# Performance work log

Hardware: AMD Instinct MI355X
Metric: run time of the kernel (lower is better)

Reference implementation:

```python
import jax, jax.numpy as jnp
import numpy as np

D_MODEL = 128
D_STATE = 256
D_CONV = 4
EXPAND = 2
D_INNER = EXPAND * D_MODEL  # 256 == D_STATE (required by the module's einsum/add)
B = 4
L = 100  # fixed: self.C has first dim 100


def silu(x):
    return x * jax.nn.sigmoid(x)


def setup_inputs() -> dict:
    key = jax.random.key(0)
    ks = jax.random.split(key, 10)
    s = 0.02
    dt_std = D_INNER ** (-0.5)
    inp = {
        "hidden_states": jax.random.normal(ks[0], (B, L, D_MODEL), jnp.float32),
        "state": jax.random.normal(ks[1], (B, L, D_INNER, D_STATE), jnp.float32),
        # torch nn.Linear layout: (out_features, in_features)
        "in_proj_w": jax.random.normal(ks[2], (2 * D_INNER, D_MODEL), jnp.float32) * s,
        "in_proj_b": jnp.zeros((2 * D_INNER,), jnp.float32),
        # depthwise conv1d weight: (d_inner, 1, d_conv)
        "conv_w": jax.random.normal(ks[3], (D_INNER, 1, D_CONV), jnp.float32) * s,
        "conv_b": jnp.zeros((D_INNER,), jnp.float32),
        "x_proj_w": jax.random.normal(ks[4], (2 * D_STATE, D_INNER), jnp.float32) * s,
        "dt_proj_w": jax.random.uniform(ks[5], (D_INNER, D_INNER), jnp.float32, -dt_std, dt_std),
        "dt_proj_b": jnp.zeros((D_INNER,), jnp.float32),
        # A_log = log(arange(1, d_state+1)) broadcast to (d_inner, d_state)
        "A_log": jnp.log(jnp.broadcast_to(jnp.arange(1, D_STATE + 1, dtype=jnp.float32), (D_INNER, D_STATE))),
        "D1": jnp.ones((D_INNER,), jnp.float32),
        # torch inits self.C to ones; add tiny noise to avoid degenerate baseline
        "C_param": jnp.ones((L, D_STATE, D_STATE), jnp.float32) + jax.random.normal(ks[6], (L, D_STATE, D_STATE), jnp.float32) * 0.01,
        "out_proj_w": jax.random.normal(ks[7], (D_MODEL, D_INNER), jnp.float32) * s,
        "out_proj_b": jnp.zeros((D_MODEL,), jnp.float32),
    }
    return inp


def reference(hidden_states, state, in_proj_w, in_proj_b, conv_w, conv_b,
              x_proj_w, dt_proj_w, dt_proj_b, A_log, D1, C_param,
              out_proj_w, out_proj_b):
    b, l, _ = hidden_states.shape
    xz = hidden_states @ in_proj_w.T + in_proj_b          # (b, l, 2*d_inner)
    x, z = jnp.split(xz, 2, axis=-1)                      # each (b, l, d_inner)

    # causal depthwise conv: pad (d_conv-1) left == conv with pad both sides then [:, :, :l]
    xc = jnp.transpose(x, (0, 2, 1))                      # (b, d_inner, l)
    xc = jax.lax.conv_general_dilated(
        xc, conv_w, window_strides=(1,), padding=[(conv_w.shape[-1] - 1, 0)],
        dimension_numbers=("NCH", "OIH", "NCH"), feature_group_count=xc.shape[1])
    xc = xc + conv_b[None, :, None]
    x = silu(jnp.transpose(xc, (0, 2, 1)))                # (b, l, d_inner)

    bc = x @ x_proj_w.T                                   # (b, l, 2*d_state)
    Bm, _Cm_unused = jnp.split(bc, 2, axis=-1)            # torch shadows chunked C with self.C

    dt = jax.nn.softplus(x @ dt_proj_w.T + dt_proj_b)     # (b, l, d_inner)
    A = -jnp.exp(A_log)                                   # (d_inner, d_state)
    dA = jnp.exp(dt[..., None] * A)                       # (b, l, d_inner, d_state)
    dB = dt[..., None] * Bm[..., None, :]                 # (b, l, d_inner, d_state)
    actual_state = state * dA + dB                        # elementwise 'blnd,blnd->blnd'

    y = jnp.einsum("bldn,ldn->bln", actual_state, C_param) + D1 * x  # (b, l, d_inner)
    y = y * silu(z)
    out = y @ out_proj_w.T + out_proj_b                   # (b, l, d_model)
    return out, actual_state
```

## Files before the change

### kernel.cpp

```cpp
#include <hip/hip_runtime.h>

#define LEN 100
#define NR 400

__device__ __forceinline__ float siluf_(float x) { return x / (1.0f + __expf(-x)); }
__device__ __forceinline__ float softplusf_(float x) {
    return (x > 20.f) ? x : log1pf(expf(x));
}

typedef float f4v __attribute__((ext_vector_type(4)));
__device__ __forceinline__ float4 nt_load4(const float* p) {
    f4v t = __builtin_nontemporal_load((const f4v*)p);
    return make_float4(t.x, t.y, t.z, t.w);
}
__device__ __forceinline__ void nt_store4(float* p, float4 v) {
    f4v t; t.x = v.x; t.y = v.y; t.z = v.z; t.w = v.w;
    __builtin_nontemporal_store(t, (f4v*)p);
}

__global__ void k_nega(const float* __restrict__ alog, float* __restrict__ negA) {
    int i = blockIdx.x * 256 + threadIdx.x;
    negA[i] = -expf(alog[i]);
}

__global__ void __launch_bounds__(256) k_front(
    const float* __restrict__ hidden, const float* __restrict__ ipw, const float* __restrict__ ipb,
    const float* __restrict__ cw, const float* __restrict__ cb,
    const float* __restrict__ xpw, const float* __restrict__ dtw, const float* __restrict__ dtb,
    float* __restrict__ xact, float* __restrict__ Bm, float* __restrict__ dt,
    float* __restrict__ zs)
{
    int r = blockIdx.x;
    int l = r % LEN;
    int j = threadIdx.x;
    int lb = l < 3 ? l : 3;
    __shared__ float hid[4][128];
    __shared__ __align__(16) float xs[256];

    for (int e = j; e < 512; e += 256) {
        int k = e >> 7;
        int c = e & 127;
        hid[k][c] = (k <= lb) ? hidden[(size_t)(r - k) * 128 + c] : 0.f;
    }
    __syncthreads();

    float b0 = ipb[j];
    float xp0 = b0, xp1 = b0, xp2 = b0, xp3 = b0;
    float z = ipb[256 + j];
    const float* wx = ipw + (size_t)j * 128;
    const float* wz = ipw + (size_t)(256 + j) * 128;
#pragma unroll 8
    for (int c = 0; c < 128; c += 4) {
        float4 w = *(const float4*)(wx + c);
        xp0 += w.x * hid[0][c] + w.y * hid[0][c+1] + w.z * hid[0][c+2] + w.w * hid[0][c+3];
        xp1 += w.x * hid[1][c] + w.y * hid[1][c+1] + w.z * hid[1][c+2] + w.w * hid[1][c+3];
        xp2 += w.x * hid[2][c] + w.y * hid[2][c+1] + w.z * hid[2][c+2] + w.w * hid[2][c+3];
        xp3 += w.x * hid[3][c] + w.y * hid[3][c+1] + w.z * hid[3][c+2] + w.w * hid[3][c+3];
        float4 v = *(const float4*)(wz + c);
        z += v.x * hid[0][c] + v.y * hid[0][c+1] + v.z * hid[0][c+2] + v.w * hid[0][c+3];
    }
    float4 w4 = *(const float4*)(cw + j * 4);
    float conv = cb[j] + w4.w * xp0;
    if (lb >= 1) conv += w4.z * xp1;
    if (lb >= 2) conv += w4.y * xp2;
    if (lb >= 3) conv += w4.x * xp3;
    float xa = siluf_(conv);
    xs[j] = xa;
    xact[r * 256 + j] = xa;
    zs[r * 256 + j] = siluf_(z);
    __syncthreads();

    float accB = 0.f, accD = dtb[j];
    const float* bw = xpw + (size_t)j * 256;
    const float* dw = dtw + (size_t)j * 256;
#pragma unroll 8
    for (int c = 0; c < 256; c += 4) {
        float4 bwv = *(const float4*)(bw + c);
        float4 dwv = *(const float4*)(dw + c);
        float4 xv  = *(const float4*)(xs + c);
        accB += bwv.x * xv.x + bwv.y * xv.y + bwv.z * xv.z + bwv.w * xv.w;
        accD += dwv.x * xv.x + dwv.y * xv.y + dwv.z * xv.z + dwv.w * xv.w;
    }
    Bm[r * 256 + j] = accB;
    dt[r * 256 + j] = softplusf_(accD);
}

__global__ void __launch_bounds__(256, 8) k_scan(
    const float* __restrict__ state, const float* __restrict__ negA,
    const float* __restrict__ Cp, const float* __restrict__ dt,
    const float* __restrict__ Bm, float* __restrict__ ostate, float* __restrict__ ypart)
{
    int bid = blockIdx.x;
    int r = bid >> 3, sl = bid & 7;
    int l = r % LEN;
    int tid = threadIdx.x;
    int wid = tid >> 6, lane = tid & 63, n0 = lane * 4;
    int d0 = sl * 32 + wid * 8;
    const float* dtp = dt + r * 256 + d0;
    float4 Bv = *(const float4*)(Bm + r * 256 + n0);
    const float* sp = state + ((size_t)(r * 256 + d0)) * 256 + n0;
    const float* cp = Cp + ((size_t)(l * 256 + d0)) * 256 + n0;
    const float* ap = negA + (size_t)d0 * 256 + n0;
    float* op = ostate + ((size_t)(r * 256 + d0)) * 256 + n0;

    __shared__ __align__(16) float accs[4][256];

    float4 acc = make_float4(0.f, 0.f, 0.f, 0.f);
    float4 s = nt_load4(sp);
    float4 c = *(const float4*)(cp);
    float4 a = *(const float4*)(ap);
#pragma unroll
    for (int i = 0; i < 8; ++i) {
        float4 s1, c1, a1;
        if (i < 7) {
            s1 = nt_load4(sp + (size_t)(i + 1) * 256);
            c1 = *(const float4*)(cp + (size_t)(i + 1) * 256);
            a1 = *(const float4*)(ap + (size_t)(i + 1) * 256);
        }
        float dtv = dtp[i];
        float4 as;
        as.x = s.x * __expf(dtv * a.x) + dtv * Bv.x;
        as.y = s.y * __expf(dtv * a.y) + dtv * Bv.y;
        as.z = s.z * __expf(dtv * a.z) + dtv * Bv.z;
        as.w = s.w * __expf(dtv * a.w) + dtv * Bv.w;
        nt_store4(op + (size_t)i * 256, as);
        acc.x += as.x * c.x;
        acc.y += as.y * c.y;
        acc.z += as.z * c.z;
        acc.w += as.w * c.w;
        if (i < 7) { s = s1; c = c1; a = a1; }
    }
    *(float4*)(&accs[wid][n0]) = acc;
    __syncthreads();
    if (wid == 0) {
        float4 t0 = *(const float4*)(&accs[0][n0]);
        float4 t1 = *(const float4*)(&accs[1][n0]);
        float4 t2 = *(const float4*)(&accs[2][n0]);
        float4 t3 = *(const float4*)(&accs[3][n0]);
        float4 o;
        o.x = t0.x + t1.x + t2.x + t3.x;
        o.y = t0.y + t1.y + t2.y + t3.y;
        o.z = t0.z + t1.z + t2.z + t3.z;
        o.w = t0.w + t1.w + t2.w + t3.w;
        *(float4*)(ypart + ((size_t)(sl * NR + r)) * 256 + n0) = o;
    }
}

__global__ void __launch_bounds__(256) k_back(
    const float* __restrict__ ypart, const float* __restrict__ xact,
    const float* __restrict__ zs, const float* __restrict__ D1,
    const float* __restrict__ ow, const float* __restrict__ ob,
    float* __restrict__ out)
{
    int r = blockIdx.x;
    int t = threadIdx.x;
    __shared__ __align__(16) float ys[256];
    const int S = NR * 256;
    int idx = r * 256 + t;
    float v = 0.f;
#pragma unroll
    for (int q = 0; q < 8; q++) v += ypart[q * S + idx];
    v += D1[t] * xact[idx];
    v *= zs[idx];
    ys[t] = v;
    __syncthreads();
    if (t < 128) {
        const float* wp = ow + (size_t)t * 256;
        float acc = ob[t];
#pragma unroll 8
        for (int c = 0; c < 256; c += 4) {
            float4 w = *(const float4*)(wp + c);
            float4 x = *(const float4*)(ys + c);
            acc += w.x * x.x + w.y * x.y + w.z * x.z + w.w * x.w;
        }
        out[r * 128 + t] = acc;
    }
}

extern "C" void kernel_launch(void* const* d_in, const int* in_sizes, int n_in,
                              void* d_out, int out_size, void* d_ws, size_t ws_size,
                              hipStream_t stream) {
    const float* hidden = (const float*)d_in[0];
    const float* state  = (const float*)d_in[1];
    const float* ipw    = (const float*)d_in[2];
    const float* ipb    = (const float*)d_in[3];
    const float* cw     = (const float*)d_in[4];
    const float* cb     = (const float*)d_in[5];
    const float* xpw    = (const float*)d_in[6];
    const float* dtw    = (const float*)d_in[7];
    const float* dtb    = (const float*)d_in[8];
    const float* alog   = (const float*)d_in[9];
    const float* D1     = (const float*)d_in[10];
    const float* Cp     = (const float*)d_in[11];
    const float* opw    = (const float*)d_in[12];
    const float* opb    = (const float*)d_in[13];

    float* out    = (float*)d_out;
    float* ostate = out + 51200;

    float* ws    = (float*)d_ws;
    float* negA  = ws;
    float* xact  = ws + 65536;
    float* Bm    = ws + 167936;
    float* dt    = ws + 270336;
    float* zs    = ws + 372736;
    float* ypart = ws + 475136;

    k_nega <<<256,  256, 0, stream>>>(alog, negA);
    k_front<<<400,  256, 0, stream>>>(hidden, ipw, ipb, cw, cb, xpw, dtw, dtb,
                                      xact, Bm, dt, zs);
    k_scan <<<3200, 256, 0, stream>>>(state, negA, Cp, dt, Bm, ostate, ypart);
    k_back <<<400,  256, 0, stream>>>(ypart, xact, zs, D1, opw, opb, out);
}
```

Baseline: 288.9 us.

## Share C_param and A loads across batch in scan kernel, drop negA kernel

The scan kernel now gives each block one sequence position and a 16-row d_inner slice, and loops over all four batch entries. Each C_param and A_log element is loaded once and reused four times instead of being reloaded for every batch. -exp(A_log) is computed inline, which removes the separate k_nega launch and its workspace buffer. This cuts C_param traffic (about 26MB) fourfold in exchange for more partial sums (16 slices) read in k_back, fewer blocks, and extra exp work per element.

```diff
diff --git a/kernel.cpp b/kernel.cpp
--- a/kernel.cpp
+++ b/kernel.cpp
@@ -16,11 +16,6 @@
 __device__ __forceinline__ void nt_store4(float* p, float4 v) {
     f4v t; t.x = v.x; t.y = v.y; t.z = v.z; t.w = v.w;
     __builtin_nontemporal_store(t, (f4v*)p);
-}
-
-__global__ void k_nega(const float* __restrict__ alog, float* __restrict__ negA) {
-    int i = blockIdx.x * 256 + threadIdx.x;
-    negA[i] = -expf(alog[i]);
 }
 
 __global__ void __launch_bounds__(256) k_front(
@@ -85,64 +80,72 @@
     dt[r * 256 + j] = softplusf_(accD);
 }
 
-__global__ void __launch_bounds__(256, 8) k_scan(
-    const float* __restrict__ state, const float* __restrict__ negA,
-    const float* __restrict__ Cp, const float* __restrict__ dt,
+__global__ void __launch_bounds__(256, 4) k_scan(
+    const float* __restrict__ state, const float* __restrict__ alog,
+    const float* __restrict__ Cp, const float* __restrict__ dtg,
     const float* __restrict__ Bm, float* __restrict__ ostate, float* __restrict__ ypart)
 {
     int bid = blockIdx.x;
-    int r = bid >> 3, sl = bid & 7;
-    int l = r % LEN;
+    int l = bid >> 4, sl = bid & 15;
     int tid = threadIdx.x;
     int wid = tid >> 6, lane = tid & 63, n0 = lane * 4;
-    int d0 = sl * 32 + wid * 8;
-    const float* dtp = dt + r * 256 + d0;
-    float4 Bv = *(const float4*)(Bm + r * 256 + n0);
-    const float* sp = state + ((size_t)(r * 256 + d0)) * 256 + n0;
+    int d0 = sl * 16 + wid * 4;
+
     const float* cp = Cp + ((size_t)(l * 256 + d0)) * 256 + n0;
-    const float* ap = negA + (size_t)d0 * 256 + n0;
-    float* op = ostate + ((size_t)(r * 256 + d0)) * 256 + n0;
-
-    __shared__ __align__(16) float accs[4][256];
-
-    float4 acc = make_float4(0.f, 0.f, 0.f, 0.f);
-    float4 s = nt_load4(sp);
-    float4 c = *(const float4*)(cp);
-    float4 a = *(const float4*)(ap);
-#pragma unroll
-    for (int i = 0; i < 8; ++i) {
-        float4 s1, c1, a1;
-        if (i < 7) {
-            s1 = nt_load4(sp + (size_t)(i + 1) * 256);
-            c1 = *(const float4*)(cp + (size_t)(i + 1) * 256);
-            a1 = *(const float4*)(ap + (size_t)(i + 1) * 256);
+    const float* ap = alog + (size_t)d0 * 256 + n0;
+
+    float4 Bv[4], dtq[4], acc[4];
+    size_t soff[4];
+#pragma unroll
+    for (int b = 0; b < 4; ++b) {
+        int r = b * LEN + l;
+        Bv[b] = *(const float4*)(Bm + r * 256 + n0);
+        dtq[b] = *(const float4*)(dtg + r * 256 + d0);
+        soff[b] = ((size_t)(r * 256 + d0)) * 256 + n0;
+        acc[b] = make_float4(0.f, 0.f, 0.f, 0.f);
+    }
+
+#pragma unroll
+    for (int i = 0; i < 4; ++i) {
+        float4 av = *(const float4*)(ap + (size_t)i * 256);
+        float4 cv = *(const float4*)(cp + (size_t)i * 256);
+        float4 na;
+        na.x = -expf(av.x); na.y = -expf(av.y);
+        na.z = -expf(av.z); na.w = -expf(av.w);
+#pragma unroll
+        for (int b = 0; b < 4; ++b) {
+            float dtv = (i == 0) ? dtq[b].x : (i == 1) ? dtq[b].y
+                      : (i == 2) ? dtq[b].z : dtq[b].w;
+            float4 s = nt_load4(state + soff[b] + (size_t)i * 256);
+            float4 as;
+            as.x = s.x * __expf(dtv * na.x) + dtv * Bv[b].x;
+            as.y = s.y * __expf(dtv * na.y) + dtv * Bv[b].y;
+            as.z = s.z * __expf(dtv * na.z) + dtv * Bv[b].z;
+            as.w = s.w * __expf(dtv * na.w) + dtv * Bv[b].w;
+            nt_store4(ostate + soff[b] + (size_t)i * 256, as);
+            acc[b].x += as.x * cv.x;
+            acc[b].y += as.y * cv.y;
+            acc[b].z += as.z * cv.z;
+            acc[b].w += as.w * cv.w;
         }
-        float dtv = dtp[i];
-        float4 as;
-        as.x = s.x * __expf(dtv * a.x) + dtv * Bv.x;
-        as.y = s.y * __expf(dtv * a.y) + dtv * Bv.y;
-        as.z = s.z * __expf(dtv * a.z) + dtv * Bv.z;
-        as.w = s.w * __expf(dtv * a.w) + dtv * Bv.w;
-        nt_store4(op + (size_t)i * 256, as);
-        acc.x += as.x * c.x;
-        acc.y += as.y * c.y;
-        acc.z += as.z * c.z;
-        acc.w += as.w * c.w;
-        if (i < 7) { s = s1; c = c1; a = a1; }
-    }
-    *(float4*)(&accs[wid][n0]) = acc;
-    __syncthreads();
-    if (wid == 0) {
-        float4 t0 = *(const float4*)(&accs[0][n0]);
-        float4 t1 = *(const float4*)(&accs[1][n0]);
-        float4 t2 = *(const float4*)(&accs[2][n0]);
-        float4 t3 = *(const float4*)(&accs[3][n0]);
+    }
+
+    __shared__ __align__(16) float accs[4][4][256];
+#pragma unroll
+    for (int b = 0; b < 4; ++b)
+        *(float4*)(&accs[wid][b][n0]) = acc[b];
+    __syncthreads();
+    {
+        float4 t0 = *(const float4*)(&accs[0][wid][n0]);
+        float4 t1 = *(const float4*)(&accs[1][wid][n0]);
+        float4 t2 = *(const float4*)(&accs[2][wid][n0]);
+        float4 t3 = *(const float4*)(&accs[3][wid][n0]);
         float4 o;
-        o.x = t0.x + t1.x + t2.x + t3.x;
-        o.y = t0.y + t1.y + t2.y + t3.y;
-        o.z = t0.z + t1.z + t2.z + t3.z;
-        o.w = t0.w + t1.w + t2.w + t3.w;
-        *(float4*)(ypart + ((size_t)(sl * NR + r)) * 256 + n0) = o;
+        o.x = (t0.x + t1.x) + (t2.x + t3.x);
+        o.y = (t0.y + t1.y) + (t2.y + t3.y);
+        o.z = (t0.z + t1.z) + (t2.z + t3.z);
+        o.w = (t0.w + t1.w) + (t2.w + t3.w);
+        *(float4*)(ypart + ((size_t)(sl * NR + wid * LEN + l)) * 256 + n0) = o;
     }
 }
 
@@ -159,7 +162,7 @@
     int idx = r * 256 + t;
     float v = 0.f;
 #pragma unroll
-    for (int q = 0; q < 8; q++) v += ypart[q * S + idx];
+    for (int q = 0; q < 16; q++) v += ypart[q * S + idx];
     v += D1[t] * xact[idx];
     v *= zs[idx];
     ys[t] = v;
@@ -199,16 +202,14 @@
     float* ostate = out + 51200;
 
     float* ws    = (float*)d_ws;
-    float* negA  = ws;
-    float* xact  = ws + 65536;
-    float* Bm    = ws + 167936;
-    float* dt    = ws + 270336;
-    float* zs    = ws + 372736;
-    float* ypart = ws + 475136;
-
-    k_nega <<<256,  256, 0, stream>>>(alog, negA);
+    float* xact  = ws;
+    float* Bm    = ws + 102400;
+    float* dt    = ws + 204800;
+    float* zs    = ws + 307200;
+    float* ypart = ws + 409600;
+
     k_front<<<400,  256, 0, stream>>>(hidden, ipw, ipb, cw, cb, xpw, dtw, dtb,
                                       xact, Bm, dt, zs);
-    k_scan <<<3200, 256, 0, stream>>>(state, negA, Cp, dt, Bm, ostate, ypart);
+    k_scan <<<1600, 256, 0, stream>>>(state, alog, Cp, dt, Bm, ostate, ypart);
     k_back <<<400,  256, 0, stream>>>(ypart, xact, zs, D1, opw, opb, out);
 }
```

Result: faster. 281.9 us (-2.4%).
